# Optimization experiments

Measured on AMD Instinct MI355X. Metric: run time of the kernel, lower is better.

The kernel has to match this reference:

```python
import jax, jax.numpy as jnp
import numpy as np

EPS = 1e-6      # eps used in token2map / map2token weight normalization
LN_EPS = 1e-5   # torch nn.LayerNorm default


def layernorm(x, w, b):
    m = jnp.mean(x, axis=-1, keepdims=True)
    xc = x - m
    v = jnp.mean(xc * xc, axis=-1, keepdims=True)
    return xc * jax.lax.rsqrt(v + LN_EPS) * w + b


def grid_index(H_init, W_init, H, W):
    # nearest-neighbor map: flattened feature-map index for each init-grid cell
    r = (jnp.arange(H_init) * H) // H_init
    c = (jnp.arange(W_init) * W) // W_init
    return (r[:, None] * W + c[None, :]).reshape(-1)  # [N_init]


def token2map(x, idx_token, H, W, H_init, W_init):
    # tokens [B,N,C] -> feature map [B,H,W,C] via weighted scatter-mean
    B, N, C = x.shape
    idx_hw = grid_index(H_init, W_init, H, W)                    # [N_init]
    counts = jnp.zeros((H * W,), x.dtype).at[idx_hw].add(1.0)    # identical across batch
    w = (1.0 / (counts + EPS))[idx_hw]                           # [N_init]
    src = jnp.take_along_axis(x, idx_token[..., None], axis=1)   # [B,N_init,C]
    out = jnp.zeros((B, H * W, C), x.dtype).at[:, idx_hw, :].add(src * w[None, :, None])
    return out.reshape(B, H, W, C)


def map2token(fmap, idx_token, N, H_init, W_init):
    # feature map [B,H,W,C] -> tokens [B,N,C]: mean of member grid cells per token
    B, H, W, C = fmap.shape
    idx_hw = grid_index(H_init, W_init, H, W)
    bidx = jnp.arange(B)[:, None]
    counts = jnp.zeros((B, N), fmap.dtype).at[bidx, idx_token].add(1.0)
    wt = jnp.take_along_axis(1.0 / (counts + EPS), idx_token, axis=1)  # [B,N_init]
    src = fmap.reshape(B, H * W, C)[:, idx_hw, :]                      # [B,N_init,C]
    return jnp.zeros((B, N, C), fmap.dtype).at[bidx, idx_token].add(src * wt[..., None])


def _forward(x, token_score, idx_token,
             norm1_w, norm1_b, q_w, q_b, kv_w, kv_b, sr_w, sr_b, srn_w, srn_b,
             proj_w, proj_b, norm2_w, norm2_b, fc1_w, fc1_b, skip_w, dw_w, dw_b,
             fc2_w, fc2_b, H, W, H_init, W_init, token_num, num_heads):
    B, N, C = x.shape
    d = C // num_heads
    scale = d ** -0.5
    sr = 2  # sr_ratio

    xn = layernorm(x, norm1_w, norm1_b)  # q_dict['x'] = norm1(x); kv_dict is q_dict

    # ---- TCFormerDynamicAttention ----
    q = (xn @ q_w + q_b).reshape(B, N, num_heads, d).transpose(0, 2, 1, 3)  # [B,h,N,d]
    tmp = jnp.concatenate([xn, token_score], axis=-1)            # [B,N,C+1]
    tmp_map = token2map(tmp, idx_token, H, W, H_init, W_init)    # [B,H,W,C+1]
    kv_map, conf_map = tmp_map[..., :C], tmp_map[..., C]
    kv = jax.lax.conv_general_dilated(kv_map, sr_w, (sr, sr), 'VALID',
        dimension_numbers=('NHWC', 'HWIO', 'NHWC')) + sr_b       # sr conv, stride 2
    M = (H // sr) * (W // sr)
    kv = layernorm(kv.reshape(B, M, C), srn_w, srn_b)
    conf = conf_map.reshape(B, H // sr, sr, W // sr, sr).mean(axis=(2, 4)).reshape(B, M)

    kv = (kv @ kv_w + kv_b).reshape(B, M, 2, num_heads, d)
    k = kv[:, :, 0].transpose(0, 2, 1, 3)                        # [B,h,M,d]
    v = kv[:, :, 1].transpose(0, 2, 1, 3)
    attn = jnp.einsum('bhnd,bhmd->bhnm', q * scale, k) + conf[:, None, None, :]
    attn = jax.nn.softmax(attn, axis=-1)
    a = jnp.einsum('bhnm,bhmd->bhnd', attn, v).transpose(0, 2, 1, 3).reshape(B, N, C)
    x = x + (a @ proj_w + proj_b)

    # ---- TCMLP ----
    h = layernorm(x, norm2_w, norm2_b) @ fc1_w + fc1_b           # [B,N,H1]
    hmap = token2map(h, idx_token, H, W, H_init, W_init)         # [B,H,W,H1]
    hmap = jax.lax.conv_general_dilated(hmap, dw_w, (1, 1), ((1, 1), (1, 1)),
        dimension_numbers=('NHWC', 'HWIO', 'NHWC'),
        feature_group_count=h.shape[-1]) + dw_b                  # depthwise 3x3
    hc = h * skip_w + map2token(hmap, idx_token, N, H_init, W_init)  # skip = dw 1x1 conv1d
    hc = jax.nn.gelu(hc, approximate=False)
    return x + (hc @ fc2_w + fc2_b)


def setup_inputs() -> dict:
    B, N, C, H1 = 8, 1568, 256, 1024
    H = W = 56
    H_init = W_init = 112
    key = jax.random.key(0)
    ks = jax.random.split(key, 16)
    r = lambda i, shape, s=0.02: jax.random.normal(ks[i], shape, jnp.float32) * s
    return {
        'x': jax.random.normal(ks[0], (B, N, C), jnp.float32),
        'token_score': jax.random.normal(ks[1], (B, N, 1), jnp.float32),
        'idx_token': jax.random.randint(ks[2], (B, H_init * W_init), 0, N),
        'norm1_w': jnp.ones((C,), jnp.float32), 'norm1_b': jnp.zeros((C,), jnp.float32),
        'q_w': r(3, (C, C)), 'q_b': jnp.zeros((C,), jnp.float32),
        'kv_w': r(4, (C, 2 * C)), 'kv_b': jnp.zeros((2 * C,), jnp.float32),
        'sr_w': r(5, (2, 2, C, C)), 'sr_b': jnp.zeros((C,), jnp.float32),
        'srn_w': jnp.ones((C,), jnp.float32), 'srn_b': jnp.zeros((C,), jnp.float32),
        'proj_w': r(6, (C, C)), 'proj_b': jnp.zeros((C,), jnp.float32),
        'norm2_w': jnp.ones((C,), jnp.float32), 'norm2_b': jnp.zeros((C,), jnp.float32),
        'fc1_w': r(7, (C, H1)), 'fc1_b': jnp.zeros((H1,), jnp.float32),
        'skip_w': 1.0 + r(8, (H1,), 0.1),
        'dw_w': r(9, (3, 3, 1, H1), 0.1), 'dw_b': jnp.zeros((H1,), jnp.float32),
        'fc2_w': r(10, (H1, C)), 'fc2_b': jnp.zeros((C,), jnp.float32),
        'H': H, 'W': W, 'H_init': H_init, 'W_init': W_init,
        'token_num': N, 'num_heads': 8,
    }


def reference(x, token_score, idx_token, norm1_w, norm1_b, q_w, q_b, kv_w, kv_b,
              sr_w, sr_b, srn_w, srn_b, proj_w, proj_b, norm2_w, norm2_b,
              fc1_w, fc1_b, skip_w, dw_w, dw_b, fc2_w, fc2_b,
              H, W, H_init, W_init, token_num, num_heads):
    return _forward(x, token_score, idx_token, norm1_w, norm1_b, q_w, q_b, kv_w, kv_b,
                    sr_w, sr_b, srn_w, srn_b, proj_w, proj_b, norm2_w, norm2_b,
                    fc1_w, fc1_b, skip_w, dw_w, dw_b, fc2_w, fc2_b,
                    H, W, H_init, W_init, token_num, num_heads)
```

## Files before the change

kernel.cpp:

```cpp
#include <hip/hip_runtime.h>
#include <math.h>

#define BB 8
#define NTOK 1568
#define CD 256
#define HIMG 56
#define WIMG 56
#define HWSZ 3136
#define HIG 112
#define WIG 112
#define NI 12544
#define MKV 784
#define MPAD 800
#define NHEADS 8
#define HEADD 32
#define HH1 1024
#define ROWS1 (BB*NTOK)
#define ROWSK (BB*MKV)
#define LOG2E 1.4426950408889634f

typedef unsigned short bfu;
typedef __attribute__((ext_vector_type(4))) unsigned short bf4;
typedef __attribute__((ext_vector_type(8))) unsigned short bf8;
typedef __attribute__((ext_vector_type(8))) short s8v;
typedef __attribute__((ext_vector_type(4))) float f4v;
typedef __attribute__((ext_vector_type(16))) float f16v;

__device__ inline float b2f(bfu u) { union { unsigned i; float f; } x; x.i = (unsigned)u << 16; return x.f; }
__device__ inline bfu f2b(float f) {
  union { float f; unsigned i; } x; x.f = f;
  unsigned r = x.i + 0x7fffu + ((x.i >> 16) & 1u);
  return (bfu)(r >> 16);
}
__device__ inline int get_isb(const unsigned* probe) { return probe[0] == 0x3F803F80u ? 1 : 0; }
__device__ inline float ldd(const void* p, size_t i, int isb) {
  return isb ? b2f(((const bfu*)p)[i]) : ((const float*)p)[i];
}
__device__ inline int xswz(int wg, int nwg) { return (wg & 7) * (nwg >> 3) + (wg >> 3); }

__global__ __launch_bounds__(256) void wtr_tile(const void* __restrict__ w0,
                                                const void* __restrict__ w1,
                                                const void* __restrict__ w2,
                                                const void* __restrict__ w3,
                                                const void* __restrict__ w4,
                                                const void* __restrict__ w5,
                                                const void* __restrict__ w6,
                                                const void* __restrict__ w7,
                                                bfu* __restrict__ wtb,
                                                const unsigned* __restrict__ probe) {
  int isb = get_isb(probe);
  int bid = blockIdx.x, tid = threadIdx.x;
  if (bid >= 1024) {
    int idx = (bid - 1024) * 256 + tid;
    if (idx < 9216) wtb[1048576 + idx] = f2b(ldd(w6, idx, isb));
    else            wtb[1048576 + idx] = f2b(ldd(w7, idx - 9216, isb));
    return;
  }
  const void* W; int K, N; bfu* Wt; int tloc;
  if (bid < 64)       { W = w0; K = 256;  N = 256;  Wt = wtb;          tloc = bid; }
  else if (bid < 320) { W = w1; K = 1024; N = 256;  Wt = wtb + 65536;  tloc = bid - 64; }
  else if (bid < 448) { W = w2; K = 256;  N = 512;  Wt = wtb + 327680; tloc = bid - 320; }
  else if (bid < 512) { W = w3; K = 256;  N = 256;  Wt = wtb + 458752; tloc = bid - 448; }
  else if (bid < 768) { W = w4; K = 256;  N = 1024; Wt = wtb + 524288; tloc = bid - 512; }
  else                { W = w5; K = 1024; N = 256;  Wt = wtb + 786432; tloc = bid - 768; }
  int ntn = N >> 5;
  int tn = tloc % ntn, tk = tloc / ntn;
  int n0 = tn * 32, k0 = tk * 32;
  __shared__ float s[32][33];
  int tx = tid & 31, ty = tid >> 5;
#pragma unroll
  for (int i = 0; i < 4; i++) {
    int k = ty + 8 * i;
    s[k][tx] = ldd(W, (size_t)(k0 + k) * N + n0 + tx, isb);
  }
  __syncthreads();
#pragma unroll
  for (int i = 0; i < 4; i++) {
    int n = ty + 8 * i;
    Wt[(size_t)(n0 + n) * K + k0 + tx] = f2b(s[tx][n]);
  }
}

__global__ __launch_bounds__(256) void ln_kernel(const void* __restrict__ in, int inmode,
                                                 const void* __restrict__ w,
                                                 const void* __restrict__ bta,
                                                 bfu* __restrict__ out,
                                                 const unsigned* __restrict__ probe) {
  int isb = get_isb(probe);
  int im = (inmode == 2) ? isb : inmode;
  int blk = xswz(blockIdx.x, gridDim.x);
  int wv = threadIdx.x >> 6, lane = threadIdx.x & 63;
  int row = blk * 4 + wv;
  int c4 = lane * 4;
  float v[4];
  if (im) {
    bf4 t = *(const bf4*)((const bfu*)in + (size_t)row * CD + c4);
#pragma unroll
    for (int j = 0; j < 4; j++) v[j] = b2f(t[j]);
  } else {
    float4 t = *(const float4*)((const float*)in + (size_t)row * CD + c4);
    v[0] = t.x; v[1] = t.y; v[2] = t.z; v[3] = t.w;
  }
  float s1 = v[0] + v[1] + v[2] + v[3];
  float s2 = v[0] * v[0] + v[1] * v[1] + v[2] * v[2] + v[3] * v[3];
#pragma unroll
  for (int off = 1; off < 64; off <<= 1) {
    s1 += __shfl_xor(s1, off);
    s2 += __shfl_xor(s2, off);
  }
  float m = s1 * (1.0f / CD);
  float inv = rsqrtf(s2 * (1.0f / CD) - m * m + 1e-5f);
  bf4 ov;
#pragma unroll
  for (int j = 0; j < 4; j++)
    ov[j] = f2b((v[j] - m) * inv * ldd(w, c4 + j, isb) + ldd(bta, c4 + j, isb));
  *(bf4*)(out + (size_t)row * CD + c4) = ov;
}

__global__ __launch_bounds__(256) void gemm_mfma(const bfu* __restrict__ A,
                                                 const bfu* __restrict__ Bt,
                                                 const void* __restrict__ bias,
                                                 const void* __restrict__ resid, int rmode,
                                                 void* __restrict__ Cc, int cmode,
                                                 void* __restrict__ aux,
                                                 int K, int Ncols,
                                                 const unsigned* __restrict__ probe) {
  int isb = get_isb(probe);
  int rm = (rmode == 1) ? (isb ? 3 : 2) : rmode;
  int cm = (cmode == 2) ? (isb ? 0 : 1) : cmode;
  __shared__ bfu As[128][40];
  __shared__ bfu Bs[128][40];
  int t = threadIdx.x;
  int wgid = xswz(blockIdx.y * gridDim.x + blockIdx.x, gridDim.x * gridDim.y);
  int bx = wgid % gridDim.x, by = wgid / gridDim.x;
  int row0 = by * 128, col0 = bx * 128;
  int sr = t >> 2, sc = (t & 3) * 8;
  int w = t >> 6, lane = t & 63;
  int wm = (w >> 1) * 64, wn = (w & 1) * 64;
  int li = lane & 15, q = lane >> 4;
  f4v zz = {0.f, 0.f, 0.f, 0.f};
  f4v acc[4][4];
#pragma unroll
  for (int mi = 0; mi < 4; mi++)
#pragma unroll
    for (int ni = 0; ni < 4; ni++) acc[mi][ni] = zz;

  for (int k0 = 0; k0 < K; k0 += 32) {
#pragma unroll
    for (int rr = sr; rr < 128; rr += 64) {
      *(s8v*)(&As[rr][sc]) = *(const s8v*)(A + (size_t)(row0 + rr) * K + k0 + sc);
      *(s8v*)(&Bs[rr][sc]) = *(const s8v*)(Bt + (size_t)(col0 + rr) * K + k0 + sc);
    }
    __syncthreads();
    s8v af[4], bf_[4];
#pragma unroll
    for (int mi = 0; mi < 4; mi++) af[mi] = *(const s8v*)(&As[wm + mi * 16 + li][q * 8]);
#pragma unroll
    for (int ni = 0; ni < 4; ni++) bf_[ni] = *(const s8v*)(&Bs[wn + ni * 16 + li][q * 8]);
#pragma unroll
    for (int mi = 0; mi < 4; mi++)
#pragma unroll
      for (int ni = 0; ni < 4; ni++)
        acc[mi][ni] = __builtin_amdgcn_mfma_f32_16x16x32_bf16(af[mi], bf_[ni], acc[mi][ni], 0, 0, 0);
    __syncthreads();
  }
  float bw[4];
#pragma unroll
  for (int ni = 0; ni < 4; ni++) bw[ni] = ldd(bias, col0 + wn + ni * 16 + li, isb);
#pragma unroll
  for (int mi = 0; mi < 4; mi++) {
#pragma unroll
    for (int ni = 0; ni < 4; ni++) {
      int col = col0 + wn + ni * 16 + li;
#pragma unroll
      for (int r = 0; r < 4; r++) {
        int row = row0 + wm + mi * 16 + q * 4 + r;
        size_t base = (size_t)row * Ncols + col;
        float v = acc[mi][ni][r] + bw[ni];
        if (rm == 2) v += ((const float*)resid)[base];
        else if (rm == 3) v += b2f(((const bfu*)resid)[base]);
        if (cm == 0) ((bfu*)Cc)[base] = f2b(v);
        else if (cm == 1) ((float*)Cc)[base] = v;
        else {
          if (col < 256) ((bfu*)Cc)[base] = f2b(v);
          else {
            int bb = row / MKV, mm = row - bb * MKV;
            ((bfu*)aux)[((size_t)(bb * 256) + (col - 256)) * MPAD + mm] = f2b(v);
          }
        }
      }
    }
  }
}

__global__ __launch_bounds__(128) void gemm64(const bfu* __restrict__ A,
                                              const bfu* __restrict__ Bt,
                                              const void* __restrict__ bias,
                                              const void* __restrict__ resid, int rmode,
                                              void* __restrict__ Cc, int cmode,
                                              void* __restrict__ aux,
                                              int K, int Ncols,
                                              const unsigned* __restrict__ probe) {
  int isb = get_isb(probe);
  int rm = (rmode == 1) ? (isb ? 3 : 2) : rmode;
  int cm = (cmode == 2) ? (isb ? 0 : 1) : cmode;
  __shared__ bfu As[64][40];
  __shared__ bfu Bs[64][40];
  int t = threadIdx.x;
  int wgid = xswz(blockIdx.y * gridDim.x + blockIdx.x, gridDim.x * gridDim.y);
  int bx = wgid % gridDim.x, by = wgid / gridDim.x;
  int row0 = by * 64, col0 = bx * 64;
  int sr = t >> 2, sc = (t & 3) * 8;
  int w = t >> 6, lane = t & 63;
  int wm = w * 32;
  int li = lane & 15, q = lane >> 4;
  f4v zz = {0.f, 0.f, 0.f, 0.f};
  f4v acc[2][4];
#pragma unroll
  for (int mi = 0; mi < 2; mi++)
#pragma unroll
    for (int ni = 0; ni < 4; ni++) acc[mi][ni] = zz;

  for (int k0 = 0; k0 < K; k0 += 32) {
#pragma unroll
    for (int rr = sr; rr < 64; rr += 32) {
      *(s8v*)(&As[rr][sc]) = *(const s8v*)(A + (size_t)(row0 + rr) * K + k0 + sc);
      *(s8v*)(&Bs[rr][sc]) = *(const s8v*)(Bt + (size_t)(col0 + rr) * K + k0 + sc);
    }
    __syncthreads();
    s8v af[2], bf_[4];
#pragma unroll
    for (int mi = 0; mi < 2; mi++) af[mi] = *(const s8v*)(&As[wm + mi * 16 + li][q * 8]);
#pragma unroll
    for (int ni = 0; ni < 4; ni++) bf_[ni] = *(const s8v*)(&Bs[ni * 16 + li][q * 8]);
#pragma unroll
    for (int mi = 0; mi < 2; mi++)
#pragma unroll
      for (int ni = 0; ni < 4; ni++)
        acc[mi][ni] = __builtin_amdgcn_mfma_f32_16x16x32_bf16(af[mi], bf_[ni], acc[mi][ni], 0, 0, 0);
    __syncthreads();
  }
  float bw[4];
#pragma unroll
  for (int ni = 0; ni < 4; ni++) bw[ni] = ldd(bias, col0 + ni * 16 + li, isb);
#pragma unroll
  for (int mi = 0; mi < 2; mi++) {
#pragma unroll
    for (int ni = 0; ni < 4; ni++) {
      int col = col0 + ni * 16 + li;
#pragma unroll
      for (int r = 0; r < 4; r++) {
        int row = row0 + wm + mi * 16 + q * 4 + r;
        size_t base = (size_t)row * Ncols + col;
        float v = acc[mi][ni][r] + bw[ni];
        if (rm == 2) v += ((const float*)resid)[base];
        else if (rm == 3) v += b2f(((const bfu*)resid)[base]);
        if (cm == 0) ((bfu*)Cc)[base] = f2b(v);
        else if (cm == 1) ((float*)Cc)[base] = v;
        else {
          if (col < 256) ((bfu*)Cc)[base] = f2b(v);
          else {
            int bb = row / MKV, mm = row - bb * MKV;
            ((bfu*)aux)[((size_t)(bb * 256) + (col - 256)) * MPAD + mm] = f2b(v);
          }
        }
      }
    }
  }
}

__global__ __launch_bounds__(256) void akv_kernel(const bfu* __restrict__ xn,
                                                  const void* __restrict__ tscore,
                                                  const int* __restrict__ idx_token,
                                                  bfu* __restrict__ Akv,
                                                  float* __restrict__ conf,
                                                  const unsigned* __restrict__ probe) {
  int isb = get_isb(probe);
  int blk = xswz(blockIdx.x, gridDim.x), tid = threadIdx.x;
  int b = blk / MKV, m = blk % MKV;
  int i2 = m / 28, j2 = m % 28;
  __shared__ int nn[16];
  __shared__ float cacc[16];
  if (tid < 16) {
    int a = (tid >> 3) & 1, kb = (tid >> 2) & 1, di = (tid >> 1) & 1, dj = tid & 1;
    int ti = 4 * i2 + 2 * a + di, tj = 4 * j2 + 2 * kb + dj;
    int n = idx_token[b * NI + ti * WIG + tj];
    nn[tid] = n;
    cacc[tid] = ldd(tscore, b * NTOK + n, isb);
  }
  __syncthreads();
  const float w4 = 1.0f / (4.0f + 1e-6f);
  int g = tid >> 6, c4 = (tid & 63) * 4;
  bf4 a0 = *(const bf4*)(xn + (size_t)(b * NTOK + nn[g * 4 + 0]) * CD + c4);
  bf4 a1 = *(const bf4*)(xn + (size_t)(b * NTOK + nn[g * 4 + 1]) * CD + c4);
  bf4 a2 = *(const bf4*)(xn + (size_t)(b * NTOK + nn[g * 4 + 2]) * CD + c4);
  bf4 a3 = *(const bf4*)(xn + (size_t)(b * NTOK + nn[g * 4 + 3]) * CD + c4);
  bf4 rv;
#pragma unroll
  for (int j = 0; j < 4; j++)
    rv[j] = f2b(w4 * (b2f(a0[j]) + b2f(a1[j]) + b2f(a2[j]) + b2f(a3[j])));
  *(bf4*)(Akv + (size_t)blk * 1024 + g * CD + c4) = rv;
  if (tid == 0) {
    float s = 0.f;
    for (int k = 0; k < 16; k++) s += cacc[k];
    conf[b * MPAD + m] = 0.25f * w4 * s * 5.656854249492381f;
  }
}

__global__ __launch_bounds__(256) void pad_kernel(bfu* __restrict__ vt, float* __restrict__ conf) {
  int t = blockIdx.x * 256 + threadIdx.x;
  int b = t / 4096, rem = t % 4096;
  int d = rem / 16, m = MKV + (rem % 16);
  vt[((size_t)(b * 256 + d)) * MPAD + m] = 0;
  if (t < 128) conf[(t / 16) * MPAD + MKV + (t % 16)] = -1e30f;
}

__global__ __launch_bounds__(256) void attn_kernel(const bfu* __restrict__ qb,
                                                   const bfu* __restrict__ kv,
                                                   const bfu* __restrict__ vt,
                                                   const float* __restrict__ conf,
                                                   bfu* __restrict__ out) {
  __shared__ float sdata[4][64][34];
  int tid = threadIdx.x;
  int w = tid >> 6, lane = tid & 63;
  int l31 = lane & 31, hi = lane >> 5;
  int blk = xswz(blockIdx.x, gridDim.x);
  int qt = blk % 25, tt = blk / 25;
  int hh = tt & 7, b = tt >> 3;
  int n0 = qt * 64;
  int two = (qt < 24);
  const bfu* qrow1 = qb + (size_t)(b * NTOK + n0 + l31) * CD + hh * HEADD + hi * 8;
  s8v qfA1 = *(const s8v*)(qrow1);
  s8v qfB1 = *(const s8v*)(qrow1 + 16);
  s8v qfA2 = {0, 0, 0, 0, 0, 0, 0, 0}, qfB2 = qfA2;
  if (two) {
    const bfu* qrow2 = qrow1 + (size_t)32 * CD;
    qfA2 = *(const s8v*)(qrow2);
    qfB2 = *(const s8v*)(qrow2 + 16);
  }
  const float scale = 0.17677669529663689f * LOG2E;
  const bfu* kbase = kv + hh * HEADD + hi * 8;
  const bfu* vbase = vt + ((size_t)(b * 256 + hh * HEADD + l31)) * MPAD + hi * 8;
  const float* cbase = conf + b * MPAD + 4 * hi;
  f16v oc1, oc2;
#pragma unroll
  for (int r = 0; r < 16; r++) { oc1[r] = 0.f; oc2[r] = 0.f; }
  float lr1 = 0.f, lr2 = 0.f;
  int w32 = w * 32;
  const bfu* kp0 = kbase + (size_t)(b * MKV + w32 + l31) * 512;
  s8v kfA = *(const s8v*)(kp0);
  s8v kfB = *(const s8v*)(kp0 + 16);
  s8v vfA = *(const s8v*)(vbase + w32);
  s8v vfB = *(const s8v*)(vbase + w32 + 16);
  float4 cf0 = *(const float4*)(cbase + w32);
  float4 cf1 = *(const float4*)(cbase + w32 + 8);
  float4 cf2 = *(const float4*)(cbase + w32 + 16);
  float4 cf3 = *(const float4*)(cbase + w32 + 24);
  for (int m0 = w32; m0 < MPAD; m0 += 128) {
    s8v ckA = kfA, ckB = kfB, cvA = vfA, cvB = vfB;
    float4 d0 = cf0, d1 = cf1, d2 = cf2, d3 = cf3;
    int m1 = m0 + 128;
    if (m1 < MPAD) {
      int mA = m1 + l31; if (mA > MKV - 1) mA = MKV - 1;
      const bfu* kp = kbase + (size_t)(b * MKV + mA) * 512;
      kfA = *(const s8v*)(kp);
      kfB = *(const s8v*)(kp + 16);
      vfA = *(const s8v*)(vbase + m1);
      vfB = *(const s8v*)(vbase + m1 + 16);
      cf0 = *(const float4*)(cbase + m1);
      cf1 = *(const float4*)(cbase + m1 + 8);
      cf2 = *(const float4*)(cbase + m1 + 16);
      cf3 = *(const float4*)(cbase + m1 + 24);
    }
    f16v cseed;
    cseed[0] = d0.x; cseed[1] = d0.y; cseed[2] = d0.z; cseed[3] = d0.w;
    cseed[4] = d1.x; cseed[5] = d1.y; cseed[6] = d1.z; cseed[7] = d1.w;
    cseed[8] = d2.x; cseed[9] = d2.y; cseed[10] = d2.z; cseed[11] = d2.w;
    cseed[12] = d3.x; cseed[13] = d3.y; cseed[14] = d3.z; cseed[15] = d3.w;
    __builtin_amdgcn_s_setprio(1);
    f16v c = __builtin_amdgcn_mfma_f32_32x32x16_bf16(ckA, qfA1, cseed, 0, 0, 0);
    c = __builtin_amdgcn_mfma_f32_32x32x16_bf16(ckB, qfB1, c, 0, 0, 0);
    __builtin_amdgcn_s_setprio(0);
    {
      float p[16], ps0 = 0.f, ps1 = 0.f, ps2 = 0.f, ps3 = 0.f;
#pragma unroll
      for (int r = 0; r < 16; r++) {
        p[r] = __builtin_amdgcn_exp2f(c[r] * scale);
        if ((r & 3) == 0) ps0 += p[r];
        else if ((r & 3) == 1) ps1 += p[r];
        else if ((r & 3) == 2) ps2 += p[r];
        else ps3 += p[r];
      }
      lr1 += (ps0 + ps1) + (ps2 + ps3);
      unsigned Z[8];
#pragma unroll
      for (int a2 = 0; a2 < 8; a2++)
        asm("v_cvt_pk_bf16_f32 %0, %1, %2" : "=v"(Z[a2]) : "v"(p[2 * a2]), "v"(p[2 * a2 + 1]));
      asm("v_permlane32_swap_b32 %0, %1" : "+v"(Z[0]), "+v"(Z[2]));
      asm("v_permlane32_swap_b32 %0, %1" : "+v"(Z[1]), "+v"(Z[3]));
      asm("v_permlane32_swap_b32 %0, %1" : "+v"(Z[4]), "+v"(Z[6]));
      asm("v_permlane32_swap_b32 %0, %1" : "+v"(Z[5]), "+v"(Z[7]));
      union { unsigned u[4]; s8v v; } B1, B2;
      B1.u[0] = Z[0]; B1.u[1] = Z[1]; B1.u[2] = Z[2]; B1.u[3] = Z[3];
      B2.u[0] = Z[4]; B2.u[1] = Z[5]; B2.u[2] = Z[6]; B2.u[3] = Z[7];
      __builtin_amdgcn_s_setprio(1);
      oc1 = __builtin_amdgcn_mfma_f32_32x32x16_bf16(cvA, B1.v, oc1, 0, 0, 0);
      oc1 = __builtin_amdgcn_mfma_f32_32x32x16_bf16(cvB, B2.v, oc1, 0, 0, 0);
      __builtin_amdgcn_s_setprio(0);
    }
    if (two) {
      __builtin_amdgcn_s_setprio(1);
      f16v c2 = __builtin_amdgcn_mfma_f32_32x32x16_bf16(ckA, qfA2, cseed, 0, 0, 0);
      c2 = __builtin_amdgcn_mfma_f32_32x32x16_bf16(ckB, qfB2, c2, 0, 0, 0);
      __builtin_amdgcn_s_setprio(0);
      float p[16], ps0 = 0.f, ps1 = 0.f, ps2 = 0.f, ps3 = 0.f;
#pragma unroll
      for (int r = 0; r < 16; r++) {
        p[r] = __builtin_amdgcn_exp2f(c2[r] * scale);
        if ((r & 3) == 0) ps0 += p[r];
        else if ((r & 3) == 1) ps1 += p[r];
        else if ((r & 3) == 2) ps2 += p[r];
        else ps3 += p[r];
      }
      lr2 += (ps0 + ps1) + (ps2 + ps3);
      unsigned Z[8];
#pragma unroll
      for (int a2 = 0; a2 < 8; a2++)
        asm("v_cvt_pk_bf16_f32 %0, %1, %2" : "=v"(Z[a2]) : "v"(p[2 * a2]), "v"(p[2 * a2 + 1]));
      asm("v_permlane32_swap_b32 %0, %1" : "+v"(Z[0]), "+v"(Z[2]));
      asm("v_permlane32_swap_b32 %0, %1" : "+v"(Z[1]), "+v"(Z[3]));
      asm("v_permlane32_swap_b32 %0, %1" : "+v"(Z[4]), "+v"(Z[6]));
      asm("v_permlane32_swap_b32 %0, %1" : "+v"(Z[5]), "+v"(Z[7]));
      union { unsigned u[4]; s8v v; } B1, B2;
      B1.u[0] = Z[0]; B1.u[1] = Z[1]; B1.u[2] = Z[2]; B1.u[3] = Z[3];
      B2.u[0] = Z[4]; B2.u[1] = Z[5]; B2.u[2] = Z[6]; B2.u[3] = Z[7];
      __builtin_amdgcn_s_setprio(1);
      oc2 = __builtin_amdgcn_mfma_f32_32x32x16_bf16(cvA, B1.v, oc2, 0, 0, 0);
      oc2 = __builtin_amdgcn_mfma_f32_32x32x16_bf16(cvB, B2.v, oc2, 0, 0, 0);
      __builtin_amdgcn_s_setprio(0);
    }
  }
#pragma unroll
  for (int r = 0; r < 16; r++) { sdata[w][lane][r] = oc1[r]; sdata[w][lane][17 + r] = oc2[r]; }
  sdata[w][lane][16] = lr1;
  sdata[w][lane][33] = lr2;
  __syncthreads();
  if (w == 0 || (w == 1 && two)) {
    int base = w * 17;
    float s[17];
#pragma unroll
    for (int r = 0; r < 17; r++)
      s[r] = sdata[0][lane][base + r] + sdata[1][lane][base + r] +
             sdata[2][lane][base + r] + sdata[3][lane][base + r];
    float l = s[16];
    l += __shfl_xor(l, 32);
    float inv = 1.0f / l;
    bfu* op = out + (size_t)(b * NTOK + n0 + w * 32 + l31) * CD + hh * HEADD + 4 * hi;
#pragma unroll
    for (int g = 0; g < 4; g++) {
      bf4 o;
#pragma unroll
      for (int u = 0; u < 4; u++) o[u] = f2b(s[4 * g + u] * inv);
      *(bf4*)(op + 8 * g) = o;
    }
  }
}

__global__ __launch_bounds__(128) void hmap_kernel(const bfu* __restrict__ h,
                                                   const int* __restrict__ idx_token,
                                                   bfu* __restrict__ hmap) {
  int blk = xswz(blockIdx.x, gridDim.x), tid = threadIdx.x;
  int b = blk / HWSZ, cell = blk % HWSZ;
  int i = cell / WIMG, j = cell % WIMG;
  __shared__ int nn[4];
  if (tid < 4) {
    int di = tid >> 1, dj = tid & 1;
    nn[tid] = idx_token[b * NI + (2 * i + di) * WIG + (2 * j + dj)];
  }
  __syncthreads();
  const float w4 = 1.0f / (4.0f + 1e-6f);
  int c8 = tid * 8;
  bf8 a0 = *(const bf8*)(h + (size_t)(b * NTOK + nn[0]) * HH1 + c8);
  bf8 a1 = *(const bf8*)(h + (size_t)(b * NTOK + nn[1]) * HH1 + c8);
  bf8 a2 = *(const bf8*)(h + (size_t)(b * NTOK + nn[2]) * HH1 + c8);
  bf8 a3 = *(const bf8*)(h + (size_t)(b * NTOK + nn[3]) * HH1 + c8);
  bf8 rv;
#pragma unroll
  for (int j2 = 0; j2 < 8; j2++)
    rv[j2] = f2b(w4 * (b2f(a0[j2]) + b2f(a1[j2]) + b2f(a2[j2]) + b2f(a3[j2])));
  *(bf8*)(hmap + (size_t)blk * HH1 + c8) = rv;
}

__global__ __launch_bounds__(256) void dw_kernel(const bfu* __restrict__ hmap,
                                                 const bfu* __restrict__ dwt,
                                                 const bfu* __restrict__ dbt,
                                                 bfu* __restrict__ dwout) {
  int blk = xswz(blockIdx.x, gridDim.x);
  int j4 = blk % 14; int rem = blk / 14;
  int i = rem % HIMG; int b = rem / HIMG;
  int tid = threadIdx.x;
  int c4 = tid * 4;
  int j0 = j4 * 4;
  float wf[9][4];
#pragma unroll
  for (int k = 0; k < 9; k++) {
    bf4 wv = *(const bf4*)(dwt + k * HH1 + c4);
#pragma unroll
    for (int u = 0; u < 4; u++) wf[k][u] = b2f(wv[u]);
  }
  bf4 bias = *(const bf4*)(dbt + c4);
  float bi[4];
#pragma unroll
  for (int u = 0; u < 4; u++) bi[u] = b2f(bias[u]);
  bf4 tp[3][6];
  const size_t bbase = (size_t)b * HWSZ;
#pragma unroll
  for (int r = 0; r < 3; r++) {
    int yy = i - 1 + r;
    bool rowok = (unsigned)yy < (unsigned)HIMG;
#pragma unroll
    for (int cc = 0; cc < 6; cc++) {
      int xx = j0 - 1 + cc;
      bf4 v = {0, 0, 0, 0};
      if (rowok && (unsigned)xx < (unsigned)WIMG)
        v = *(const bf4*)(hmap + (bbase + yy * WIMG + xx) * HH1 + c4);
      tp[r][cc] = v;
    }
  }
#pragma unroll
  for (int j = 0; j < 4; j++) {
    float acc[4] = {bi[0], bi[1], bi[2], bi[3]};
#pragma unroll
    for (int r = 0; r < 3; r++)
#pragma unroll
      for (int kx = 0; kx < 3; kx++) {
        bf4 hv = tp[r][j + kx];
#pragma unroll
        for (int u = 0; u < 4; u++) acc[u] += b2f(hv[u]) * wf[r * 3 + kx][u];
      }
    bf4 ov;
#pragma unroll
    for (int u = 0; u < 4; u++) ov[u] = f2b(acc[u]);
    *(bf4*)(dwout + (bbase + i * WIMG + j0 + j) * HH1 + c4) = ov;
  }
}

__global__ void zero_int(int* p) { p[blockIdx.x * 256 + threadIdx.x] = 0; }
__global__ void count_kernel(const int* __restrict__ idx, int* __restrict__ cnt) {
  int t = xswz(blockIdx.x, gridDim.x) * 256 + threadIdx.x;
  int b = t / NI;
  atomicAdd(&cnt[b * NTOK + idx[t]], 1);
}
__global__ __launch_bounds__(256) void scan_kernel(const int* __restrict__ cnt, int* __restrict__ offs) {
  int b = blockIdx.x, tid = threadIdx.x;
  __shared__ int s[NTOK];
  for (int i = tid; i < NTOK; i += 256) s[i] = cnt[b * NTOK + i];
  __syncthreads();
  for (int st = 1; st < NTOK; st <<= 1) {
    int vals[7]; int k = 0;
    for (int i = tid; i < NTOK; i += 256, k++) vals[k] = (i >= st) ? s[i - st] : 0;
    __syncthreads();
    k = 0;
    for (int i = tid; i < NTOK; i += 256, k++) s[i] += vals[k];
    __syncthreads();
  }
  for (int i = tid; i < NTOK; i += 256) offs[b * NTOK + i] = (i > 0) ? s[i - 1] : 0;
}
__global__ void fill_kernel(const int* __restrict__ idx, const int* __restrict__ offs,
                            int* __restrict__ cursor, int* __restrict__ tlist) {
  int t = xswz(blockIdx.x, gridDim.x) * 256 + threadIdx.x;
  int b = t / NI, tt = t % NI;
  int n = idx[t];
  int p = atomicAdd(&cursor[b * NTOK + n], 1);
  tlist[b * NI + offs[b * NTOK + n] + p] = tt;
}

__global__ __launch_bounds__(128) void m2t_kernel(const bfu* __restrict__ h,
                                                  const bfu* __restrict__ dwout,
                                                  const int* __restrict__ cnt,
                                                  const int* __restrict__ offs,
                                                  const int* __restrict__ tlist,
                                                  const void* __restrict__ skipw,
                                                  bfu* __restrict__ hc,
                                                  const unsigned* __restrict__ probe) {
  int isb = get_isb(probe);
  int blk = xswz(blockIdx.x, gridDim.x), tid = threadIdx.x;
  int b = blk / NTOK, n = blk % NTOK;
  int c = cnt[b * NTOK + n];
  int o0 = offs[b * NTOK + n];
  float inv = 1.0f / ((float)c + 1e-6f);
  int c8 = tid * 8;
  float a[8] = {};
  for (int k = 0; k < c; k++) {
    int tt = tlist[b * NI + o0 + k];
    int ti = tt / WIG, tj = tt % WIG;
    int cell = (ti >> 1) * WIMG + (tj >> 1);
    bf8 dv = *(const bf8*)(dwout + ((size_t)b * HWSZ + cell) * HH1 + c8);
#pragma unroll
    for (int j2 = 0; j2 < 8; j2++) a[j2] += b2f(dv[j2]);
  }
  bf8 hv = *(const bf8*)(h + (size_t)blk * HH1 + c8);
  bf8 ov;
  const float is2 = 0.70710678118654752f;
#pragma unroll
  for (int j2 = 0; j2 < 8; j2++) {
    float r = b2f(hv[j2]) * ldd(skipw, c8 + j2, isb) + a[j2] * inv;
    r = 0.5f * r * (1.0f + erff(r * is2));
    ov[j2] = f2b(r);
  }
  *(bf8*)(hc + (size_t)blk * HH1 + c8) = ov;
}

extern "C" void kernel_launch(void* const* d_in, const int* in_sizes, int n_in,
                              void* d_out, int out_size, void* d_ws, size_t ws_size,
                              hipStream_t stream) {
  const void* x        = d_in[0];
  const void* tscore   = d_in[1];
  const int*  idx_tok  = (const int*)d_in[2];
  const void* norm1_w  = d_in[3];
  const void* norm1_b  = d_in[4];
  const void* q_w      = d_in[5];
  const void* q_b      = d_in[6];
  const void* kv_w     = d_in[7];
  const void* kv_b     = d_in[8];
  const void* sr_w     = d_in[9];
  const void* sr_b     = d_in[10];
  const void* srn_w    = d_in[11];
  const void* srn_b    = d_in[12];
  const void* proj_w   = d_in[13];
  const void* proj_b   = d_in[14];
  const void* norm2_w  = d_in[15];
  const void* norm2_b  = d_in[16];
  const void* fc1_w    = d_in[17];
  const void* fc1_b    = d_in[18];
  const void* skip_w   = d_in[19];
  const void* dw_w     = d_in[20];
  const void* dw_b     = d_in[21];
  const void* fc2_w    = d_in[22];
  const void* fc2_b    = d_in[23];
  const unsigned* probe = (const unsigned*)d_in[3];

  float* ws = (float*)d_ws;
  size_t o = 0;
  float* x2 = ws + o;          o += (size_t)ROWS1 * CD;
  float* hR = ws + o;          o += (size_t)ROWS1 * HH1 / 2;
  float* mR = ws + o;          o += (size_t)BB * HWSZ * HH1 / 2;
  float* dR = ws + o;          o += (size_t)BB * HWSZ * HH1 / 2;
  int* ibase = (int*)(ws + o); o += (size_t)(3 * ROWS1 + BB * NI);
  bfu* wtb   = (bfu*)(ws + o); o += 529408;
  bfu* vtb   = (bfu*)(ws + o);

  bfu* Akv   = (bfu*)hR;
  bfu* kvc   = (bfu*)(hR + (size_t)ROWSK * 1024 / 2);
  bfu* h     = (bfu*)hR;
  bfu* qbuf  = (bfu*)mR;
  bfu* kvout = (bfu*)(mR + (size_t)ROWS1 * CD / 2);
  float* conf  = mR + (size_t)ROWS1 * CD / 2 + (size_t)ROWSK * 512 / 2;
  bfu* hmap  = (bfu*)mR;
  bfu* hc    = (bfu*)mR;
  bfu* xn    = (bfu*)dR;
  bfu* dwout = (bfu*)dR;
  int* counts = ibase;
  int* cursor = ibase + ROWS1;
  int* offs   = ibase + 2 * ROWS1;
  int* tlist  = ibase + 3 * ROWS1;
  bfu* q_wt    = wtb;
  bfu* sr_wt   = wtb + 65536;
  bfu* kv_wt   = wtb + 327680;
  bfu* proj_wt = wtb + 458752;
  bfu* fc1_wt  = wtb + 524288;
  bfu* fc2_wt  = wtb + 786432;
  bfu* dwt     = wtb + 1048576;
  bfu* dbt     = wtb + 1057792;

  wtr_tile<<<1064, 256, 0, stream>>>(q_w, sr_w, kv_w, proj_w, fc1_w, fc2_w, dw_w, dw_b, wtb, probe);
  pad_kernel<<<128, 256, 0, stream>>>(vtb, conf);

  ln_kernel<<<ROWS1 / 4, 256, 0, stream>>>(x, 2, norm1_w, norm1_b, xn, probe);
  gemm64<<<dim3(4, 196), 128, 0, stream>>>(xn, q_wt, q_b, nullptr, 0, qbuf, 0, nullptr, 256, 256, probe);
  akv_kernel<<<ROWSK, 256, 0, stream>>>(xn, tscore, idx_tok, Akv, conf, probe);
  gemm64<<<dim3(4, 98), 128, 0, stream>>>(Akv, sr_wt, sr_b, nullptr, 0, kvc, 0, nullptr, 1024, 256, probe);
  ln_kernel<<<ROWSK / 4, 256, 0, stream>>>(kvc, 1, srn_w, srn_b, kvc, probe);
  gemm64<<<dim3(8, 98), 128, 0, stream>>>(kvc, kv_wt, kv_b, nullptr, 0, kvout, 3, vtb, 256, 512, probe);
  attn_kernel<<<BB * NHEADS * 25, 256, 0, stream>>>(qbuf, kvout, vtb, conf, xn);
  gemm64<<<dim3(4, 196), 128, 0, stream>>>(xn, proj_wt, proj_b, x, 1, x2, 1, nullptr, 256, 256, probe);
  ln_kernel<<<ROWS1 / 4, 256, 0, stream>>>(x2, 0, norm2_w, norm2_b, xn, probe);
  gemm_mfma<<<dim3(8, 98), 256, 0, stream>>>(xn, fc1_wt, fc1_b, nullptr, 0, h, 0, nullptr, 256, 1024, probe);
  hmap_kernel<<<BB * HWSZ, 128, 0, stream>>>(h, idx_tok, hmap);
  dw_kernel<<<BB * HIMG * 14, 256, 0, stream>>>(hmap, dwt, dbt, dwout);
  zero_int<<<(2 * ROWS1) / 256, 256, 0, stream>>>(counts);
  count_kernel<<<(BB * NI) / 256, 256, 0, stream>>>(idx_tok, counts);
  scan_kernel<<<BB, 256, 0, stream>>>(counts, offs);
  fill_kernel<<<(BB * NI) / 256, 256, 0, stream>>>(idx_tok, offs, cursor, tlist);
  m2t_kernel<<<ROWS1, 128, 0, stream>>>(h, dwout, counts, offs, tlist, skip_w, hc, probe);
  gemm64<<<dim3(4, 196), 128, 0, stream>>>(hc, fc2_wt, fc2_b, x2, 2, d_out, 2, nullptr, 1024, 256, probe);
}
```

Measured before the change: 446.1 us.

## Replace LDS-staged GEMMs with register-direct 32x32 MFMA GEMM

```diff
diff --git a/kernel.cpp b/kernel.cpp
--- a/kernel.cpp
+++ b/kernel.cpp
@@ -23,7 +23,6 @@
 typedef __attribute__((ext_vector_type(4))) unsigned short bf4;
 typedef __attribute__((ext_vector_type(8))) unsigned short bf8;
 typedef __attribute__((ext_vector_type(8))) short s8v;
-typedef __attribute__((ext_vector_type(4))) float f4v;
 typedef __attribute__((ext_vector_type(16))) float f16v;
 
 __device__ inline float b2f(bfu u) { union { unsigned i; float f; } x; x.i = (unsigned)u << 16; return x.f; }
@@ -36,7 +35,9 @@
 __device__ inline float ldd(const void* p, size_t i, int isb) {
   return isb ? b2f(((const bfu*)p)[i]) : ((const float*)p)[i];
 }
-__device__ inline int xswz(int wg, int nwg) { return (wg & 7) * (nwg >> 3) + (wg >> 3); }
+__device__ inline int xswz(int wg, int nwg) {
+  return (nwg & 7) ? wg : (wg & 7) * (nwg >> 3) + (wg >> 3);
+}
 
 __global__ __launch_bounds__(256) void wtr_tile(const void* __restrict__ w0,
                                                 const void* __restrict__ w1,
@@ -117,154 +118,66 @@
   *(bf4*)(out + (size_t)row * CD + c4) = ov;
 }
 
-__global__ __launch_bounds__(256) void gemm_mfma(const bfu* __restrict__ A,
-                                                 const bfu* __restrict__ Bt,
-                                                 const void* __restrict__ bias,
-                                                 const void* __restrict__ resid, int rmode,
-                                                 void* __restrict__ Cc, int cmode,
-                                                 void* __restrict__ aux,
-                                                 int K, int Ncols,
-                                                 const unsigned* __restrict__ probe) {
+__global__ __launch_bounds__(256) void rgemm(const bfu* __restrict__ A,
+                                             const bfu* __restrict__ Bt,
+                                             const void* __restrict__ bias,
+                                             const void* __restrict__ resid, int rmode,
+                                             void* __restrict__ Cc, int cmode,
+                                             void* __restrict__ aux,
+                                             int K, int Ncols,
+                                             const unsigned* __restrict__ probe) {
   int isb = get_isb(probe);
   int rm = (rmode == 1) ? (isb ? 3 : 2) : rmode;
   int cm = (cmode == 2) ? (isb ? 0 : 1) : cmode;
-  __shared__ bfu As[128][40];
-  __shared__ bfu Bs[128][40];
-  int t = threadIdx.x;
-  int wgid = xswz(blockIdx.y * gridDim.x + blockIdx.x, gridDim.x * gridDim.y);
-  int bx = wgid % gridDim.x, by = wgid / gridDim.x;
-  int row0 = by * 128, col0 = bx * 128;
-  int sr = t >> 2, sc = (t & 3) * 8;
-  int w = t >> 6, lane = t & 63;
-  int wm = (w >> 1) * 64, wn = (w & 1) * 64;
-  int li = lane & 15, q = lane >> 4;
-  f4v zz = {0.f, 0.f, 0.f, 0.f};
-  f4v acc[4][4];
-#pragma unroll
-  for (int mi = 0; mi < 4; mi++)
-#pragma unroll
-    for (int ni = 0; ni < 4; ni++) acc[mi][ni] = zz;
-
-  for (int k0 = 0; k0 < K; k0 += 32) {
-#pragma unroll
-    for (int rr = sr; rr < 128; rr += 64) {
-      *(s8v*)(&As[rr][sc]) = *(const s8v*)(A + (size_t)(row0 + rr) * K + k0 + sc);
-      *(s8v*)(&Bs[rr][sc]) = *(const s8v*)(Bt + (size_t)(col0 + rr) * K + k0 + sc);
+  int nbx = Ncols >> 6;
+  int id = xswz(blockIdx.x, gridDim.x);
+  int bx = id % nbx, by = id / nbx;
+  int w = threadIdx.x >> 6, lane = threadIdx.x & 63;
+  int l31 = lane & 31, hi = lane >> 5;
+  int m0 = by * 128 + w * 32;
+  int c0 = bx * 64;
+  const bfu* pa  = A  + (size_t)(m0 + l31) * K + hi * 8;
+  const bfu* pb0 = Bt + (size_t)(c0 + l31) * K + hi * 8;
+  const bfu* pb1 = Bt + (size_t)(c0 + 32 + l31) * K + hi * 8;
+  f16v acc0, acc1;
+#pragma unroll
+  for (int r = 0; r < 16; r++) { acc0[r] = 0.f; acc1[r] = 0.f; }
+  s8v aA  = *(const s8v*)(pa),       b0A = *(const s8v*)(pb0),      b1A = *(const s8v*)(pb1);
+  s8v aB  = *(const s8v*)(pa + 16),  b0B = *(const s8v*)(pb0 + 16), b1B = *(const s8v*)(pb1 + 16);
+  for (int k0 = 32; k0 <= K; k0 += 32) {
+    s8v caA = aA, cb0A = b0A, cb1A = b1A, caB = aB, cb0B = b0B, cb1B = b1B;
+    if (k0 < K) {
+      aA  = *(const s8v*)(pa + k0);       b0A = *(const s8v*)(pb0 + k0);      b1A = *(const s8v*)(pb1 + k0);
+      aB  = *(const s8v*)(pa + k0 + 16);  b0B = *(const s8v*)(pb0 + k0 + 16); b1B = *(const s8v*)(pb1 + k0 + 16);
     }
-    __syncthreads();
-    s8v af[4], bf_[4];
-#pragma unroll
-    for (int mi = 0; mi < 4; mi++) af[mi] = *(const s8v*)(&As[wm + mi * 16 + li][q * 8]);
-#pragma unroll
-    for (int ni = 0; ni < 4; ni++) bf_[ni] = *(const s8v*)(&Bs[wn + ni * 16 + li][q * 8]);
-#pragma unroll
-    for (int mi = 0; mi < 4; mi++)
-#pragma unroll
-      for (int ni = 0; ni < 4; ni++)
-        acc[mi][ni] = __builtin_amdgcn_mfma_f32_16x16x32_bf16(af[mi], bf_[ni], acc[mi][ni], 0, 0, 0);
-    __syncthreads();
-  }
-  float bw[4];
-#pragma unroll
-  for (int ni = 0; ni < 4; ni++) bw[ni] = ldd(bias, col0 + wn + ni * 16 + li, isb);
-#pragma unroll
-  for (int mi = 0; mi < 4; mi++) {
-#pragma unroll
-    for (int ni = 0; ni < 4; ni++) {
-      int col = col0 + wn + ni * 16 + li;
-#pragma unroll
-      for (int r = 0; r < 4; r++) {
-        int row = row0 + wm + mi * 16 + q * 4 + r;
-        size_t base = (size_t)row * Ncols + col;
-        float v = acc[mi][ni][r] + bw[ni];
-        if (rm == 2) v += ((const float*)resid)[base];
-        else if (rm == 3) v += b2f(((const bfu*)resid)[base]);
-        if (cm == 0) ((bfu*)Cc)[base] = f2b(v);
-        else if (cm == 1) ((float*)Cc)[base] = v;
-        else {
-          if (col < 256) ((bfu*)Cc)[base] = f2b(v);
-          else {
-            int bb = row / MKV, mm = row - bb * MKV;
-            ((bfu*)aux)[((size_t)(bb * 256) + (col - 256)) * MPAD + mm] = f2b(v);
-          }
-        }
-      }
-    }
-  }
-}
-
-__global__ __launch_bounds__(128) void gemm64(const bfu* __restrict__ A,
-                                              const bfu* __restrict__ Bt,
-                                              const void* __restrict__ bias,
-                                              const void* __restrict__ resid, int rmode,
-                                              void* __restrict__ Cc, int cmode,
-                                              void* __restrict__ aux,
-                                              int K, int Ncols,
-                                              const unsigned* __restrict__ probe) {
-  int isb = get_isb(probe);
-  int rm = (rmode == 1) ? (isb ? 3 : 2) : rmode;
-  int cm = (cmode == 2) ? (isb ? 0 : 1) : cmode;
-  __shared__ bfu As[64][40];
-  __shared__ bfu Bs[64][40];
-  int t = threadIdx.x;
-  int wgid = xswz(blockIdx.y * gridDim.x + blockIdx.x, gridDim.x * gridDim.y);
-  int bx = wgid % gridDim.x, by = wgid / gridDim.x;
-  int row0 = by * 64, col0 = bx * 64;
-  int sr = t >> 2, sc = (t & 3) * 8;
-  int w = t >> 6, lane = t & 63;
-  int wm = w * 32;
-  int li = lane & 15, q = lane >> 4;
-  f4v zz = {0.f, 0.f, 0.f, 0.f};
-  f4v acc[2][4];
-#pragma unroll
-  for (int mi = 0; mi < 2; mi++)
-#pragma unroll
-    for (int ni = 0; ni < 4; ni++) acc[mi][ni] = zz;
-
-  for (int k0 = 0; k0 < K; k0 += 32) {
-#pragma unroll
-    for (int rr = sr; rr < 64; rr += 32) {
-      *(s8v*)(&As[rr][sc]) = *(const s8v*)(A + (size_t)(row0 + rr) * K + k0 + sc);
-      *(s8v*)(&Bs[rr][sc]) = *(const s8v*)(Bt + (size_t)(col0 + rr) * K + k0 + sc);
-    }
-    __syncthreads();
-    s8v af[2], bf_[4];
-#pragma unroll
-    for (int mi = 0; mi < 2; mi++) af[mi] = *(const s8v*)(&As[wm + mi * 16 + li][q * 8]);
-#pragma unroll
-    for (int ni = 0; ni < 4; ni++) bf_[ni] = *(const s8v*)(&Bs[ni * 16 + li][q * 8]);
-#pragma unroll
-    for (int mi = 0; mi < 2; mi++)
-#pragma unroll
-      for (int ni = 0; ni < 4; ni++)
-        acc[mi][ni] = __builtin_amdgcn_mfma_f32_16x16x32_bf16(af[mi], bf_[ni], acc[mi][ni], 0, 0, 0);
-    __syncthreads();
-  }
-  float bw[4];
-#pragma unroll
-  for (int ni = 0; ni < 4; ni++) bw[ni] = ldd(bias, col0 + ni * 16 + li, isb);
-#pragma unroll
-  for (int mi = 0; mi < 2; mi++) {
-#pragma unroll
-    for (int ni = 0; ni < 4; ni++) {
-      int col = col0 + ni * 16 + li;
-#pragma unroll
-      for (int r = 0; r < 4; r++) {
-        int row = row0 + wm + mi * 16 + q * 4 + r;
-        size_t base = (size_t)row * Ncols + col;
-        float v = acc[mi][ni][r] + bw[ni];
-        if (rm == 2) v += ((const float*)resid)[base];
-        else if (rm == 3) v += b2f(((const bfu*)resid)[base]);
-        if (cm == 0) ((bfu*)Cc)[base] = f2b(v);
-        else if (cm == 1) ((float*)Cc)[base] = v;
-        else {
-          if (col < 256) ((bfu*)Cc)[base] = f2b(v);
-          else {
-            int bb = row / MKV, mm = row - bb * MKV;
-            ((bfu*)aux)[((size_t)(bb * 256) + (col - 256)) * MPAD + mm] = f2b(v);
-          }
-        }
-      }
+    __builtin_amdgcn_s_setprio(1);
+    acc0 = __builtin_amdgcn_mfma_f32_32x32x16_bf16(caA, cb0A, acc0, 0, 0, 0);
+    acc1 = __builtin_amdgcn_mfma_f32_32x32x16_bf16(caA, cb1A, acc1, 0, 0, 0);
+    acc0 = __builtin_amdgcn_mfma_f32_32x32x16_bf16(caB, cb0B, acc0, 0, 0, 0);
+    acc1 = __builtin_amdgcn_mfma_f32_32x32x16_bf16(caB, cb1B, acc1, 0, 0, 0);
+    __builtin_amdgcn_s_setprio(0);
+  }
+  float bw0 = ldd(bias, c0 + l31, isb);
+  float bw1 = ldd(bias, c0 + 32 + l31, isb);
+#pragma unroll
+  for (int r = 0; r < 16; r++) {
+    int row = m0 + (r & 3) + 8 * (r >> 2) + 4 * hi;
+    size_t base0 = (size_t)row * Ncols + c0 + l31;
+    size_t base1 = base0 + 32;
+    float v0 = acc0[r] + bw0;
+    float v1 = acc1[r] + bw1;
+    if (rm == 2) { v0 += ((const float*)resid)[base0]; v1 += ((const float*)resid)[base1]; }
+    else if (rm == 3) { v0 += b2f(((const bfu*)resid)[base0]); v1 += b2f(((const bfu*)resid)[base1]); }
+    if (cm == 0) { ((bfu*)Cc)[base0] = f2b(v0); ((bfu*)Cc)[base1] = f2b(v1); }
+    else if (cm == 1) { ((float*)Cc)[base0] = v0; ((float*)Cc)[base1] = v1; }
+    else {
+      int bb = row / MKV, mm = row - bb * MKV;
+      int col0c = c0 + l31;
+      if (col0c < 256) ((bfu*)Cc)[base0] = f2b(v0);
+      else ((bfu*)aux)[((size_t)(bb * 256) + (col0c - 256)) * MPAD + mm] = f2b(v0);
+      int col1c = col0c + 32;
+      if (col1c < 256) ((bfu*)Cc)[base1] = f2b(v1);
+      else ((bfu*)aux)[((size_t)(bb * 256) + (col1c - 256)) * MPAD + mm] = f2b(v1);
     }
   }
 }
@@ -677,15 +590,15 @@
   pad_kernel<<<128, 256, 0, stream>>>(vtb, conf);
 
   ln_kernel<<<ROWS1 / 4, 256, 0, stream>>>(x, 2, norm1_w, norm1_b, xn, probe);
-  gemm64<<<dim3(4, 196), 128, 0, stream>>>(xn, q_wt, q_b, nullptr, 0, qbuf, 0, nullptr, 256, 256, probe);
+  rgemm<<<392, 256, 0, stream>>>(xn, q_wt, q_b, nullptr, 0, qbuf, 0, nullptr, 256, 256, probe);
   akv_kernel<<<ROWSK, 256, 0, stream>>>(xn, tscore, idx_tok, Akv, conf, probe);
-  gemm64<<<dim3(4, 98), 128, 0, stream>>>(Akv, sr_wt, sr_b, nullptr, 0, kvc, 0, nullptr, 1024, 256, probe);
+  rgemm<<<196, 256, 0, stream>>>(Akv, sr_wt, sr_b, nullptr, 0, kvc, 0, nullptr, 1024, 256, probe);
   ln_kernel<<<ROWSK / 4, 256, 0, stream>>>(kvc, 1, srn_w, srn_b, kvc, probe);
-  gemm64<<<dim3(8, 98), 128, 0, stream>>>(kvc, kv_wt, kv_b, nullptr, 0, kvout, 3, vtb, 256, 512, probe);
+  rgemm<<<392, 256, 0, stream>>>(kvc, kv_wt, kv_b, nullptr, 0, kvout, 3, vtb, 256, 512, probe);
   attn_kernel<<<BB * NHEADS * 25, 256, 0, stream>>>(qbuf, kvout, vtb, conf, xn);
-  gemm64<<<dim3(4, 196), 128, 0, stream>>>(xn, proj_wt, proj_b, x, 1, x2, 1, nullptr, 256, 256, probe);
+  rgemm<<<392, 256, 0, stream>>>(xn, proj_wt, proj_b, x, 1, x2, 1, nullptr, 256, 256, probe);
   ln_kernel<<<ROWS1 / 4, 256, 0, stream>>>(x2, 0, norm2_w, norm2_b, xn, probe);
-  gemm_mfma<<<dim3(8, 98), 256, 0, stream>>>(xn, fc1_wt, fc1_b, nullptr, 0, h, 0, nullptr, 256, 1024, probe);
+  rgemm<<<1568, 256, 0, stream>>>(xn, fc1_wt, fc1_b, nullptr, 0, h, 0, nullptr, 256, 1024, probe);
   hmap_kernel<<<BB * HWSZ, 128, 0, stream>>>(h, idx_tok, hmap);
   dw_kernel<<<BB * HIMG * 14, 256, 0, stream>>>(hmap, dwt, dbt, dwout);
   zero_int<<<(2 * ROWS1) / 256, 256, 0, stream>>>(counts);
@@ -693,5 +606,5 @@
   scan_kernel<<<BB, 256, 0, stream>>>(counts, offs);
   fill_kernel<<<(BB * NI) / 256, 256, 0, stream>>>(idx_tok, offs, cursor, tlist);
   m2t_kernel<<<ROWS1, 128, 0, stream>>>(h, dwout, counts, offs, tlist, skip_w, hc, probe);
-  gemm64<<<dim3(4, 196), 128, 0, stream>>>(hc, fc2_wt, fc2_b, x2, 2, d_out, 2, nullptr, 1024, 256, probe);
-}
+  rgemm<<<392, 256, 0, stream>>>(hc, fc2_wt, fc2_b, x2, 2, d_out, 2, nullptr, 1024, 256, probe);
+}
```

New measurement: 482.6 us. 1.08x slower.
